# Kernel tuning notes

Measured on AMD Instinct MI355X. Metric: run time of the kernel, lower is better.

The kernel has to match this reference:

```python
import jax, jax.numpy as jnp
import numpy as np
from functools import partial

N = 100000
E = 1600000
F_IN, F_HID, F_OUT = 128, 128, 64


def setup_inputs() -> dict:
    key = jax.random.key(0)
    ks = jax.random.split(key, 10)
    x = jax.random.normal(ks[0], (N, F_IN), dtype=jnp.float32)
    edge_index = jax.random.randint(ks[1], (2, E), 0, N, dtype=jnp.int64)
    edge_attr = jax.random.uniform(ks[2], (E,), dtype=jnp.float32)
    # GCNConv params: Linear(in, out, bias=False) weight + separate bias
    def glorot(k, fan_in, fan_out):
        lim = jnp.sqrt(6.0 / (fan_in + fan_out))
        return jax.random.uniform(k, (fan_in, fan_out), minval=-lim, maxval=lim, dtype=jnp.float32)
    return {
        "x": x, "edge_index": edge_index, "edge_attr": edge_attr,
        "W1": glorot(ks[3], F_IN, F_HID),  "b1": jnp.zeros((F_HID,), jnp.float32),
        "W2": glorot(ks[4], F_HID, F_HID), "b2": jnp.zeros((F_HID,), jnp.float32),
        "W3": glorot(ks[5], F_HID, F_OUT), "b3": jnp.zeros((F_OUT,), jnp.float32),
    }


def _gcn_norm(src, dst, ew, n):
    # PyG gcn_norm: add self-loops with weight 1, symmetric normalization.
    loop = jnp.arange(n, dtype=src.dtype)
    src_f = jnp.concatenate([src, loop])
    dst_f = jnp.concatenate([dst, loop])
    ew_f = jnp.concatenate([ew, jnp.ones((n,), ew.dtype)])
    deg = jax.ops.segment_sum(ew_f, dst_f, num_segments=n)
    dinv = jnp.where(deg > 0, jax.lax.rsqrt(deg), 0.0)
    norm = dinv[src_f] * ew_f * dinv[dst_f]  # [E+N]
    return src_f, dst_f, norm


def _gcn_conv(x, W, b, src_f, dst_f, norm, n):
    h = x @ W  # [N, out]
    msg = norm[:, None] * h[src_f]  # gather + per-edge scale
    out = jax.ops.segment_sum(msg, dst_f, num_segments=n)  # scatter-add
    return out + b


def reference(x, edge_index, edge_attr, W1, b1, W2, b2, W3, b3):
    n = x.shape[0]
    src, dst = edge_index[0], edge_index[1]
    src_f, dst_f, norm = _gcn_norm(src, dst, edge_attr, n)
    h = jax.nn.relu(_gcn_conv(x, W1, b1, src_f, dst_f, norm, n))
    h = jax.nn.relu(_gcn_conv(h, W2, b2, src_f, dst_f, norm, n))
    out = _gcn_conv(h, W3, b3, src_f, dst_f, norm, n)
    return jax.nn.log_softmax(out, axis=-1)
```

## Files before the change

kernel.cpp:

```cpp
#include <hip/hip_runtime.h>

typedef unsigned short ushortT;
typedef unsigned int uintT;
typedef unsigned long long ullT;
typedef __attribute__((ext_vector_type(8))) short bf16x8;
typedef __attribute__((ext_vector_type(4))) float f32x4;

#define NBUCK 391
#define EPB   4096
#define NBEB  391
#define BSLOT 4608

union H16 { ushortT u; _Float16 h; };

__device__ __forceinline__ float bf2f(uintT u16) {
    return __uint_as_float(u16 << 16);
}
__device__ __forceinline__ float bflo(uintT u) {
    return __uint_as_float(u << 16);
}
__device__ __forceinline__ float bfhi(uintT u) {
    return __uint_as_float(u & 0xffff0000u);
}
__device__ __forceinline__ ushortT f2bf(float f) {
    unsigned int u = __float_as_uint(f);
    unsigned int r = (u + 0x7fffu + ((u >> 16) & 1u)) >> 16;
    return (ushortT)r;
}

#define ACC8(U, W) \
    acc[0] = fmaf(W, bflo(U.x), acc[0]); acc[1] = fmaf(W, bfhi(U.x), acc[1]); \
    acc[2] = fmaf(W, bflo(U.y), acc[2]); acc[3] = fmaf(W, bfhi(U.y), acc[3]); \
    acc[4] = fmaf(W, bflo(U.z), acc[4]); acc[5] = fmaf(W, bfhi(U.z), acc[5]); \
    acc[6] = fmaf(W, bflo(U.w), acc[6]); acc[7] = fmaf(W, bfhi(U.w), acc[7]);


__device__ __forceinline__ void twist_body(const float* W, ushortT* Wt, int K, int C, int idx) {
    if (idx < K * C) {
        int k = idx / C, c = idx - k * C;
        Wt[c * K + k] = f2bf(W[idx]);
    }
}

template <int C, bool ABF16>
__device__ __forceinline__ void gemm_body(const void* Aop, const ushortT* Wt,
                                          ushortT* outp, int nrows, int bid, int tid) {
    const int K = 128;
    int wv = tid >> 6;
    int ln = tid & 63;
    int row0 = (bid * 4 + wv) * 16;
    if (row0 >= nrows) return;
    int rA = ln & 15;
    int kg = ln >> 4;
    int rowA = row0 + rA;
    bool okA = rowA < nrows;

    bf16x8 af[4];
    if (ABF16) {
        const ushortT* A = (const ushortT*)Aop;
        #pragma unroll
        for (int kb = 0; kb < 4; ++kb) {
            if (okA) af[kb] = *(const bf16x8*)(A + (size_t)rowA * K + kb * 32 + kg * 8);
            else     af[kb] = (bf16x8)(short)0;
        }
    } else {
        const float* A = (const float*)Aop;
        #pragma unroll
        for (int kb = 0; kb < 4; ++kb) {
            bf16x8 t = (bf16x8)(short)0;
            if (okA) {
                const float4* ap = reinterpret_cast<const float4*>(A + (size_t)rowA * K + kb * 32 + kg * 8);
                float4 p0 = ap[0], p1 = ap[1];
                t[0] = (short)f2bf(p0.x); t[1] = (short)f2bf(p0.y);
                t[2] = (short)f2bf(p0.z); t[3] = (short)f2bf(p0.w);
                t[4] = (short)f2bf(p1.x); t[5] = (short)f2bf(p1.y);
                t[6] = (short)f2bf(p1.z); t[7] = (short)f2bf(p1.w);
            }
            af[kb] = t;
        }
    }

    int colB = ln & 15;
    f32x4 acc[C / 16];
    #pragma unroll
    for (int nt = 0; nt < C / 16; ++nt) acc[nt] = (f32x4)0.0f;
    #pragma unroll
    for (int nt = 0; nt < C / 16; ++nt) {
        int c = nt * 16 + colB;
        #pragma unroll
        for (int kb = 0; kb < 4; ++kb) {
            bf16x8 bfr = *(const bf16x8*)(Wt + c * K + kb * 32 + kg * 8);
            acc[nt] = __builtin_amdgcn_mfma_f32_16x16x32_bf16(af[kb], bfr, acc[nt], 0, 0, 0);
        }
    }
    #pragma unroll
    for (int nt = 0; nt < C / 16; ++nt) {
        #pragma unroll
        for (int r = 0; r < 4; ++r) {
            int rowC = row0 + (ln >> 4) * 4 + r;
            if (rowC < nrows) outp[(size_t)rowC * C + nt * 16 + colB] = f2bf(acc[nt][r]);
        }
    }
}

__global__ __launch_bounds__(512) void k_sort_twist(const int* src, const int* dst, const float* ew,
                                                    int* bucket_count, ullT* erec, int e,
                                                    const float* W1, ushortT* Wt1,
                                                    const float* W2, ushortT* Wt2,
                                                    const float* W3, ushortT* Wt3) {
    __shared__ ullT srec[EPB];
    __shared__ int  gaddr[EPB];
    __shared__ int  hist[512];
    __shared__ int  adj[NBUCK];
    int blk = blockIdx.x, t = threadIdx.x;
    if (blk >= NBEB) {
        int tb = blk - NBEB;
        if (tb < 32)      twist_body(W1, Wt1, 128, 128, tb * 512 + t);
        else if (tb < 64) twist_body(W2, Wt2, 128, 128, (tb - 32) * 512 + t);
        else              twist_body(W3, Wt3, 128, 64, (tb - 64) * 512 + t);
        return;
    }
    hist[t] = 0;
    __syncthreads();
    int base = blk * EPB;
    for (int j = t; j < EPB; j += 512) {
        int i = base + j;
        if (i < e) atomicAdd(&hist[dst[i] >> 8], 1);
    }
    __syncthreads();
    int myc = hist[t];
    for (int off = 1; off < 512; off <<= 1) {
        int x = 0; if (t >= off) x = hist[t - off];
        __syncthreads();
        if (t >= off) hist[t] += x;
        __syncthreads();
    }
    int lb = (t == 0) ? 0 : hist[t - 1];
    __syncthreads();
    hist[t] = lb;
    if (t < NBUCK) {
        int gb = 0;
        if (myc > 0) gb = atomicAdd(&bucket_count[t], myc);
        adj[t] = t * BSLOT + gb - lb;
    }
    __syncthreads();
    for (int j = t; j < EPB; j += 512) {
        int i = base + j;
        if (i < e) {
            int d = dst[i];
            int b = d >> 8;
            int pos = atomicAdd(&hist[b], 1);
            H16 cv; cv.h = (_Float16)ew[i];
            ullT rec = ((ullT)(uintT)src[i] << 24) | ((ullT)(uintT)(d & 255) << 16) | (ullT)cv.u;
            srec[pos] = rec;
            int ga = adj[b] + pos;
            int lim = b * BSLOT + BSLOT - 1;
            gaddr[pos] = ga <= lim ? ga : lim;
        }
    }
    __syncthreads();
    int m = e - base; if (m > EPB) m = EPB;
    for (int k = t; k < m; k += 512) {
        erec[(size_t)gaddr[k]] = srec[k];
    }
}

__global__ __launch_bounds__(256) void k_bucket_gemm1(const ullT* erec,
                                                      const int* bucket_count,
                                                      uintT* entries, float* dinv, int* counts, int n,
                                                      const float* x, const ushortT* Wt1,
                                                      ushortT* hw1) {
    __shared__ int cnt[256];
    __shared__ uintT wsum[256];
    int blk = blockIdx.x, t = threadIdx.x;
    if (blk < NBUCK) {
        int b = blk;
        cnt[t] = 0; wsum[t] = 0;
        __syncthreads();
        int beg = b * BSLOT, m = bucket_count[b];
        if (m > BSLOT) m = BSLOT;
        for (int j = t; j < m; j += 256) {
            ullT rec = erec[(size_t)beg + j];
            int dlow = (int)((rec >> 16) & 255);
            ushortT hu = (ushortT)(rec & 0xffffu);
            int slot = atomicAdd(&cnt[dlow], 1);
            H16 cv; cv.u = hu;
            atomicAdd(&wsum[dlow], (uintT)__float2uint_rn((float)cv.h * 16777216.0f));
            if (slot < 64) {
                uintT s = (uintT)(rec >> 24);
                entries[((size_t)b * 256 + dlow) * 64 + slot] = (s << 15) | (uintT)hu;
            }
        }
        __syncthreads();
        int node = b * 256 + t;
        if (node < n) {
            float sum = (float)wsum[t] * (1.0f / 16777216.0f);
            dinv[node] = rsqrtf(1.0f + sum);
            int c = cnt[t];
            counts[node] = c > 64 ? 64 : c;
        }
    } else {
        gemm_body<128, false>(x, Wt1, hw1, n, blk - NBUCK, t);
    }
}

template <int C, bool ABF16>
__global__ __launch_bounds__(256) void k_gemm(const void* Aop, const ushortT* Wt,
                                              ushortT* outp, int nrows) {
    gemm_body<C, ABF16>(Aop, Wt, outp, nrows, blockIdx.x, threadIdx.x);
}

__global__ __launch_bounds__(256) void k_agg128(const char* hwb, const float* dinv,
                                                const int* counts, const uintT* entries,
                                                const float* bias, uintT* outp, int n) {
    __shared__ ullT wp[4][64];
    int wv = threadIdx.x >> 6, ln = threadIdx.x & 63;
    int i = blockIdx.x * 4 + wv;
    if (i >= n) return;
    int lg = ln & 15;
    int gp = ln >> 4;

    float wfac = dinv[i];
    int cnt = counts[i];
    int cntp = (cnt + 7) & ~7;
    uintT ent = entries[(size_t)i * 64 + ln];
    int s_l = (ln < cnt) ? (int)(ent >> 15) : 0;
    H16 cv; cv.u = (ushortT)(ent & 0x7fffu);
    float w_l = (ln < cnt) ? dinv[s_l] * (float)cv.h * wfac : 0.f;
    wp[wv][ln] = ((ullT)__float_as_uint(w_l) << 32) | (ullT)((uintT)s_l << 8);
    const ullT* wpw = wp[wv];

    const char* lane_base = hwb + (size_t)(lg * 16);
    uint4 uself = *(const uint4*)(lane_base + (size_t)i * 256);

    float acc[8];
    #pragma unroll
    for (int j = 0; j < 8; ++j) acc[j] = 0.f;

    ullT pa = wpw[gp], pb = wpw[4 + gp];
    uint4 ua = *(const uint4*)(lane_base + (uintT)pa);
    uint4 ub = *(const uint4*)(lane_base + (uintT)pb);
    for (int e = 8; e < cntp; e += 8) {
        ullT pa2 = wpw[e + gp], pb2 = wpw[e + 4 + gp];
        uint4 ua2 = *(const uint4*)(lane_base + (uintT)pa2);
        uint4 ub2 = *(const uint4*)(lane_base + (uintT)pb2);
        float wa = __uint_as_float((uintT)(pa >> 32));
        float wb = __uint_as_float((uintT)(pb >> 32));
        ACC8(ua, wa)
        ACC8(ub, wb)
        pa = pa2; pb = pb2; ua = ua2; ub = ub2;
    }
    {
        float wa = __uint_as_float((uintT)(pa >> 32));
        float wb = __uint_as_float((uintT)(pb >> 32));
        ACC8(ua, wa)
        ACC8(ub, wb)
    }

    #pragma unroll
    for (int j = 0; j < 8; ++j) {
        acc[j] += __shfl_xor(acc[j], 16);
        acc[j] += __shfl_xor(acc[j], 32);
    }
    float selfw = wfac * wfac;
    ACC8(uself, selfw)

    float a0 = (gp & 1) ? ((gp & 2) ? acc[6] : acc[2]) : ((gp & 2) ? acc[4] : acc[0]);
    float a1 = (gp & 1) ? ((gp & 2) ? acc[7] : acc[3]) : ((gp & 2) ? acc[5] : acc[1]);
    float2 bs = *(const float2*)(bias + (lg * 8 + gp * 2));
    a0 = fmaxf(a0 + bs.x, 0.f);
    a1 = fmaxf(a1 + bs.y, 0.f);
    outp[(size_t)i * 64 + (lg * 4 + gp)] = (uintT)f2bf(a0) | ((uintT)f2bf(a1) << 16);
}

__global__ __launch_bounds__(256) void k_agg_softmax(const char* hwb, const float* dinv,
                                                     const int* counts, const uintT* entries,
                                                     const float* bias, float* outp, int n) {
    __shared__ ullT wp[4][64];
    int wv = threadIdx.x >> 6, ln = threadIdx.x & 63;
    int i = blockIdx.x * 4 + wv;
    if (i >= n) return;
    int lg = ln & 7;
    int gp = ln >> 3;

    float wfac = dinv[i];
    int cnt = counts[i];
    int cntp = (cnt + 7) & ~7;
    uintT ent = entries[(size_t)i * 64 + ln];
    int s_l = (ln < cnt) ? (int)(ent >> 15) : 0;
    H16 cv; cv.u = (ushortT)(ent & 0x7fffu);
    float w_l = (ln < cnt) ? dinv[s_l] * (float)cv.h * wfac : 0.f;
    wp[wv][ln] = ((ullT)__float_as_uint(w_l) << 32) | (ullT)((uintT)s_l << 7);
    const ullT* wpw = wp[wv];

    const char* lane_base = hwb + (size_t)(lg * 16);
    uint4 uself = *(const uint4*)(lane_base + (size_t)i * 128);

    float acc[8];
    #pragma unroll
    for (int j = 0; j < 8; ++j) acc[j] = 0.f;

    ullT pa = wpw[gp];
    uint4 ua = *(const uint4*)(lane_base + (uintT)pa);
    for (int e = 8; e < cntp; e += 8) {
        ullT pa2 = wpw[e + gp];
        uint4 ua2 = *(const uint4*)(lane_base + (uintT)pa2);
        float wa = __uint_as_float((uintT)(pa >> 32));
        ACC8(ua, wa)
        pa = pa2; ua = ua2;
    }
    {
        float wa = __uint_as_float((uintT)(pa >> 32));
        ACC8(ua, wa)
    }

    #pragma unroll
    for (int j = 0; j < 8; ++j) {
        acc[j] += __shfl_xor(acc[j], 8);
        acc[j] += __shfl_xor(acc[j], 16);
        acc[j] += __shfl_xor(acc[j], 32);
    }
    float selfw = wfac * wfac;
    ACC8(uself, selfw)

    float4 bsa = *(const float4*)(bias + lg * 8);
    float4 bsb = *(const float4*)(bias + lg * 8 + 4);
    acc[0] += bsa.x; acc[1] += bsa.y; acc[2] += bsa.z; acc[3] += bsa.w;
    acc[4] += bsb.x; acc[5] += bsb.y; acc[6] += bsb.z; acc[7] += bsb.w;

    float m = acc[0];
    #pragma unroll
    for (int j = 1; j < 8; ++j) m = fmaxf(m, acc[j]);
    m = fmaxf(m, __shfl_xor(m, 1));
    m = fmaxf(m, __shfl_xor(m, 2));
    m = fmaxf(m, __shfl_xor(m, 4));
    float s = 0.f;
    #pragma unroll
    for (int j = 0; j < 8; ++j) s += __expf(acc[j] - m);
    s += __shfl_xor(s, 1);
    s += __shfl_xor(s, 2);
    s += __shfl_xor(s, 4);
    float ls = m + __logf(s);

    float v0 = (gp & 1) ? acc[4] : acc[0];
    float v1 = (gp & 1) ? acc[5] : acc[1];
    float v2 = (gp & 1) ? acc[6] : acc[2];
    float v3 = (gp & 1) ? acc[7] : acc[3];
    if (gp < 2) {
        float4 r = { v0 - ls, v1 - ls, v2 - ls, v3 - ls };
        *(float4*)(outp + (size_t)i * 64 + lg * 8 + gp * 4) = r;
    }
}

extern "C" void kernel_launch(void* const* d_in, const int* in_sizes, int n_in,
                              void* d_out, int out_size, void* d_ws, size_t ws_size,
                              hipStream_t stream) {
    const int N = 100000, E = 1600000;
    const int NPAD = NBUCK * 256;
    const float* x  = (const float*)d_in[0];
    const int*   src = (const int*)d_in[1];
    const int*   dst = src + E;
    const float* ea = (const float*)d_in[2];
    const float* W1 = (const float*)d_in[3];
    const float* b1 = (const float*)d_in[4];
    const float* W2 = (const float*)d_in[5];
    const float* b2 = (const float*)d_in[6];
    const float* W3 = (const float*)d_in[7];
    const float* b3 = (const float*)d_in[8];
    float* outp = (float*)d_out;

    char* ws = (char*)d_ws;
    auto alloc = [&](size_t bytes) {
        char* p = ws;
        ws += (bytes + 255) & ~(size_t)255;
        return p;
    };
    int*   bucket_count = (int*)alloc((size_t)NBUCK * 4);
    ullT*  erec         = (ullT*)alloc((size_t)NBUCK * BSLOT * 8);
    float* dinv    = (float*)alloc((size_t)N * 4);
    int*   counts  = (int*)  alloc((size_t)N * 4);
    uintT* entries = (uintT*)alloc((size_t)NPAD * 64 * 4);
    ushortT* Wt1   = (ushortT*)alloc(128 * 128 * 2);
    ushortT* Wt2   = (ushortT*)alloc(128 * 128 * 2);
    ushortT* Wt3   = (ushortT*)alloc(128 * 64 * 2);
    ushortT* hwA   = (ushortT*)alloc((size_t)N * 128 * 2);
    ushortT* hwB   = (ushortT*)alloc((size_t)N * 128 * 2);

    const int nbGemm = (N + 63) / 64;
    const int nbAgg  = (N + 3) / 4;

    hipMemsetAsync(bucket_count, 0, (size_t)NBUCK * 4, stream);
    k_sort_twist<<<NBEB + 80, 512, 0, stream>>>(src, dst, ea, bucket_count, erec, E,
                                                W1, Wt1, W2, Wt2, W3, Wt3);
    k_bucket_gemm1<<<NBUCK + nbGemm, 256, 0, stream>>>(erec, bucket_count,
                                                       entries, dinv, counts, N,
                                                       x, Wt1, hwA);
    k_agg128<<<nbAgg, 256, 0, stream>>>((const char*)hwA, dinv, counts, entries,
                                        b1, (uintT*)hwB, N);
    k_gemm<128, true><<<nbGemm, 256, 0, stream>>>(hwB, Wt2, hwA, N);
    k_agg128<<<nbAgg, 256, 0, stream>>>((const char*)hwA, dinv, counts, entries,
                                        b2, (uintT*)hwB, N);
    k_gemm<64, true><<<nbGemm, 256, 0, stream>>>(hwB, Wt3, hwA, N);
    k_agg_softmax<<<nbAgg, 256, 0, stream>>>((const char*)hwA, dinv, counts, entries,
                                             b3, outp, N);
}
```

Baseline: 405.6 us.

## Fuse aggregation with following layer GEMM via LDS-staged MFMA tile

Merges the layer-1/2 neighbor aggregation kernels with the next layer's weight GEMM. Each 1024-thread block aggregates 16 nodes (one wave per node) and writes the bf16 rows into swizzled LDS. A subset of waves then multiplies that 16-row tile by the transposed weights with 16x16x32 bf16 MFMA. This removes the intermediate activation write/read round trip and two launches. The cost is a block-wide barrier, idle waves during the GEMM, and Wt reloaded from global by every block. The bounds check is dropped, which relies on N being divisible by 16.

```diff
diff --git a/kernel.cpp b/kernel.cpp
--- a/kernel.cpp
+++ b/kernel.cpp
@@ -204,19 +204,15 @@
     }
 }
 
-template <int C, bool ABF16>
-__global__ __launch_bounds__(256) void k_gemm(const void* Aop, const ushortT* Wt,
-                                              ushortT* outp, int nrows) {
-    gemm_body<C, ABF16>(Aop, Wt, outp, nrows, blockIdx.x, threadIdx.x);
-}
-
-__global__ __launch_bounds__(256) void k_agg128(const char* hwb, const float* dinv,
-                                                const int* counts, const uintT* entries,
-                                                const float* bias, uintT* outp, int n) {
-    __shared__ ullT wp[4][64];
+template <int C>
+__global__ __launch_bounds__(1024) void k_agg_gemm(const char* hwb, const float* dinv,
+                                                   const int* counts, const uintT* entries,
+                                                   const float* bias, const ushortT* Wt,
+                                                   ushortT* outp, int n) {
+    __shared__ ullT wp[16][64];
+    __shared__ uintT rows[16][64];
     int wv = threadIdx.x >> 6, ln = threadIdx.x & 63;
-    int i = blockIdx.x * 4 + wv;
-    if (i >= n) return;
+    int i = blockIdx.x * 16 + wv;
     int lg = ln & 15;
     int gp = ln >> 4;
 
@@ -267,10 +263,40 @@
 
     float a0 = (gp & 1) ? ((gp & 2) ? acc[6] : acc[2]) : ((gp & 2) ? acc[4] : acc[0]);
     float a1 = (gp & 1) ? ((gp & 2) ? acc[7] : acc[3]) : ((gp & 2) ? acc[5] : acc[1]);
-    float2 bs = *(const float2*)(bias + (lg * 8 + gp * 2));
+    int d = lg * 4 + gp;
+    float2 bs = *(const float2*)(bias + 2 * d);
     a0 = fmaxf(a0 + bs.x, 0.f);
     a1 = fmaxf(a1 + bs.y, 0.f);
-    outp[(size_t)i * 64 + (lg * 4 + gp)] = (uintT)f2bf(a0) | ((uintT)f2bf(a1) << 16);
+    uintT packed = (uintT)f2bf(a0) | ((uintT)f2bf(a1) << 16);
+    rows[wv][((d * 4) ^ ((wv & 7) << 4)) >> 2] = packed;
+    __syncthreads();
+
+    if (wv < C / 16) {
+        int nt = wv;
+        int rA = ln & 15;
+        int kg = ln >> 4;
+        int colB = ln & 15;
+        const char* rbase = (const char*)&rows[0][0];
+        bf16x8 af[4];
+        #pragma unroll
+        for (int kb = 0; kb < 4; ++kb) {
+            int byteoff = (kb * 64 + kg * 16) ^ ((rA & 7) << 4);
+            af[kb] = *(const bf16x8*)(rbase + rA * 256 + byteoff);
+        }
+        f32x4 gac = (f32x4)0.0f;
+        int c = nt * 16 + colB;
+        #pragma unroll
+        for (int kb = 0; kb < 4; ++kb) {
+            bf16x8 bfr = *(const bf16x8*)(Wt + c * 128 + kb * 32 + kg * 8);
+            gac = __builtin_amdgcn_mfma_f32_16x16x32_bf16(af[kb], bfr, gac, 0, 0, 0);
+        }
+        int row0 = blockIdx.x * 16;
+        #pragma unroll
+        for (int r = 0; r < 4; ++r) {
+            int rowC = row0 + kg * 4 + r;
+            outp[(size_t)rowC * C + nt * 16 + colB] = f2bf(gac[r]);
+        }
+    }
 }
 
 __global__ __launch_bounds__(256) void k_agg_softmax(const char* hwb, const float* dinv,
@@ -387,6 +413,7 @@
     ushortT* hwB   = (ushortT*)alloc((size_t)N * 128 * 2);
 
     const int nbGemm = (N + 63) / 64;
+    const int nbFused = N / 16;
     const int nbAgg  = (N + 3) / 4;
 
     hipMemsetAsync(bucket_count, 0, (size_t)NBUCK * 4, stream);
@@ -395,12 +422,10 @@
     k_bucket_gemm1<<<NBUCK + nbGemm, 256, 0, stream>>>(erec, bucket_count,
                                                        entries, dinv, counts, N,
                                                        x, Wt1, hwA);
-    k_agg128<<<nbAgg, 256, 0, stream>>>((const char*)hwA, dinv, counts, entries,
-                                        b1, (uintT*)hwB, N);
-    k_gemm<128, true><<<nbGemm, 256, 0, stream>>>(hwB, Wt2, hwA, N);
-    k_agg128<<<nbAgg, 256, 0, stream>>>((const char*)hwA, dinv, counts, entries,
-                                        b2, (uintT*)hwB, N);
-    k_gemm<64, true><<<nbGemm, 256, 0, stream>>>(hwB, Wt3, hwA, N);
+    k_agg_gemm<128><<<nbFused, 1024, 0, stream>>>((const char*)hwA, dinv, counts, entries,
+                                                  b1, Wt2, hwB, N);
+    k_agg_gemm<64><<<nbFused, 1024, 0, stream>>>((const char*)hwB, dinv, counts, entries,
+                                                 b2, Wt3, hwA, N);
     k_agg_softmax<<<nbAgg, 256, 0, stream>>>((const char*)hwA, dinv, counts, entries,
                                              b3, outp, N);
 }
```

Measured after the change: 370.7 us. -8.6%, faster.
